# Kernel tuning notes

Measured on AMD Instinct MI355X. Metric: run time of the kernel, lower is better.

The kernel has to match this reference:

```python
import jax, jax.numpy as jnp
import numpy as np

NUM_HEADS = 32
HEAD_DIM = 128
HIDDEN = 4096
SEQ = 2048
BATCH = 1


def rotate_half(x):
    x1, x2 = jnp.split(x, 2, axis=-1)
    return jnp.concatenate((-x2, x1), axis=-1)


def rope_cos_sin(seq_len, dim, dtype=jnp.float32):
    inv_freq = 1.0 / (10000.0 ** (jnp.arange(0, dim, 2, dtype=jnp.float32) / dim))
    t = jnp.arange(seq_len, dtype=jnp.float32)
    freqs = jnp.einsum('i,j->ij', t, inv_freq)          # [S, dim/2]
    emb = jnp.concatenate((freqs, freqs), axis=-1)       # [S, dim]
    return jnp.cos(emb).astype(dtype), jnp.sin(emb).astype(dtype)


def setup_inputs() -> dict:
    key = jax.random.key(0)
    ks = jax.random.split(key, 6)
    s = 1.0 / np.sqrt(HIDDEN)
    return {
        'hidden_states': jax.random.normal(ks[0], (BATCH, SEQ, HIDDEN), jnp.float32),
        'attention_mask': jnp.ones((BATCH, SEQ), jnp.int32),
        'Wq': jax.random.normal(ks[1], (HIDDEN, HIDDEN), jnp.float32) * s,
        'Wk': jax.random.normal(ks[2], (HIDDEN, HIDDEN), jnp.float32) * s,
        'Wv': jax.random.normal(ks[3], (HIDDEN, HIDDEN), jnp.float32) * s,
        'Wo': jax.random.normal(ks[4], (HIDDEN, HIDDEN), jnp.float32) * s,
        'latent_queries': jax.random.normal(ks[5], (1, SEQ, HIDDEN), jnp.float32) * s,
    }


def reference(hidden_states, attention_mask, Wq, Wk, Wv, Wo, latent_queries):
    B, S, H = hidden_states.shape
    hd = HEAD_DIM
    scaling = hd ** -0.5

    def split_heads(x):  # [B,S,H] -> [B,nh,S,hd]
        return x.reshape(B, S, NUM_HEADS, hd).transpose(0, 2, 1, 3)

    k = split_heads(hidden_states @ Wk.T)
    v = split_heads(hidden_states @ Wv.T)

    cos, sin = rope_cos_sin(S, hd, hidden_states.dtype)  # [S,hd]
    cos = cos[None, None]
    sin = sin[None, None]
    k = k * cos + rotate_half(k) * sin  # rotated q is dead code in the original

    latents = jnp.broadcast_to(latent_queries[:, :S, :], (B, S, H))
    latent_q = split_heads(latents @ Wq.T)

    scores = jnp.einsum('bhqd,bhkd->bhqk', latent_q, k) * scaling
    mask = attention_mask[:, None, None, :] == 0
    scores = jnp.where(mask, -jnp.inf, scores)
    attn = jax.nn.softmax(scores.astype(jnp.float32), axis=-1).astype(hidden_states.dtype)
    # dropout is identity in eval mode
    out = jnp.einsum('bhqk,bhkd->bhqd', attn, v)
    out = out.transpose(0, 2, 1, 3).reshape(B, S, H)
    return out @ Wo.T
```

## Files before the change

### kernel.cpp

```cpp
#include <hip/hip_runtime.h>
#include <cstdint>
#include <type_traits>

typedef short bf16x8 __attribute__((ext_vector_type(8)));
typedef float f32x4 __attribute__((ext_vector_type(4)));

__device__ __forceinline__ ushort f2bf(float f) {
  union { float f; uint32_t u; } v; v.f = f;
  return (ushort)((v.u + 0x7fffu + ((v.u >> 16) & 1u)) >> 16);
}
__device__ __forceinline__ float bf2f(ushort u) {
  union { uint32_t u; float f; } v; v.u = ((uint32_t)u) << 16;
  return v.f;
}
__device__ __forceinline__ uint32_t pkbf(float x, float y) {
  uint32_t ux = (__float_as_uint(x) + 0x8000u) >> 16;
  uint32_t uy = (__float_as_uint(y) + 0x8000u) & 0xffff0000u;
  return ux | uy;
}

__device__ __forceinline__ void gld16(const void* g, void* l) {
  __builtin_amdgcn_global_load_lds(
      (__attribute__((address_space(1))) void*)(g),
      (__attribute__((address_space(3))) void*)(l), 16, 0, 0);
}

__device__ __forceinline__ uint4 ld8(const ushort* p) { return *(const uint4*)p; }
__device__ __forceinline__ uint4 ld8(const float* p) {
  float4 a = *(const float4*)p;
  float4 b = *(const float4*)(p + 4);
  uint4 r;
  r.x = pkbf(a.x, a.y); r.y = pkbf(a.z, a.w);
  r.z = pkbf(b.x, b.y); r.w = pkbf(b.z, b.w);
  return r;
}

__global__ __launch_bounds__(256) void cvt_bf16(
    const float* __restrict__ src, ushort* __restrict__ dst, int n8)
{
  int i = blockIdx.x * 256 + threadIdx.x;
  if (i >= n8) return;
  const float4* s = (const float4*)src;
  float4 a = s[2 * i], b = s[2 * i + 1];
  uint4 r;
  r.x = pkbf(a.x, a.y); r.y = pkbf(a.z, a.w);
  r.z = pkbf(b.x, b.y); r.w = pkbf(b.z, b.w);
  ((uint4*)dst)[i] = r;
}


#define BARw() __builtin_amdgcn_s_barrier()
#define LGKMW() do { asm volatile("s_waitcnt lgkmcnt(0)" ::: "memory"); \
                     __builtin_amdgcn_sched_barrier(0); } while (0)
#define VM6() asm volatile("s_waitcnt vmcnt(6)" ::: "memory")
#define VM0() asm volatile("s_waitcnt vmcnt(0)" ::: "memory")

__device__ __forceinline__ void stage_half8(
    const ushort* __restrict__ G, int row0, int col0,
    ushort* lds, int wave, int r4, int c8s)
{
#pragma unroll
  for (int q = 0; q < 2; ++q) {
    const int si = q * 8 + wave;
    const ushort* g = G + (size_t)(row0 + (si >> 1) * 16 + r4) * 4096
                        + (col0 + (si & 1) * 32 + c8s);
    gld16(g, lds + si * 512);
  }
}

__device__ __forceinline__ void read_a8(const ushort* base, int wm, int l16,
                                        int qsw, bf16x8 (&a)[4][2])
{
#pragma unroll
  for (int f = 0; f < 4; ++f)
#pragma unroll
    for (int ks = 0; ks < 2; ++ks)
      a[f][ks] = *(const bf16x8*)(base + ((wm * 4 + f) * 2 + ks) * 512
                                       + l16 * 32 + qsw);
}

__device__ __forceinline__ void read_b8(const ushort* base, int wn, int l16,
                                        int qsw, bf16x8 (&b)[2][2])
{
#pragma unroll
  for (int f = 0; f < 2; ++f)
#pragma unroll
    for (int ks = 0; ks < 2; ++ks)
      b[f][ks] = *(const bf16x8*)(base + ((wn * 2 + f) * 2 + ks) * 512
                                       + l16 * 32 + qsw);
}

template <int MH, int NH>
__device__ __forceinline__ void mfma_quad(const bf16x8 (&a)[4][2],
                                          const bf16x8 (&b)[2][2],
                                          f32x4 (&acc)[8][4])
{
  __builtin_amdgcn_s_setprio(1);
#pragma unroll
  for (int ks = 0; ks < 2; ++ks)
#pragma unroll
    for (int f = 0; f < 4; ++f)
#pragma unroll
      for (int g = 0; g < 2; ++g)
        acc[MH * 4 + f][NH * 2 + g] = __builtin_amdgcn_mfma_f32_16x16x32_bf16(
            a[f][ks], b[g][ks], acc[MH * 4 + f][NH * 2 + g], 0, 0, 0);
  __builtin_amdgcn_s_setprio(0);
}

template <int NT, int MODE>
__global__ __launch_bounds__(512, 2) void gemm8(
    const ushort* __restrict__ A0, const ushort* __restrict__ A1,
    const ushort* __restrict__ B0, const ushort* __restrict__ B1,
    ushort* __restrict__ O0, ushort* __restrict__ O1, ushort* __restrict__ O2,
    float* __restrict__ PF)
{
  __shared__ __align__(16) ushort smem[65536];
#define LDSA(P, H) (smem + (P) * 32768 + (H) * 8192)
#define LDSB(P, H) (smem + (P) * 32768 + 16384 + (H) * 8192)

  const int tid  = threadIdx.x;
  const int wave = tid >> 6;
  const int lane = tid & 63;
  const int quad = lane >> 4;
  const int l16  = lane & 15;
  const int wm   = wave >> 2;
  const int wn   = wave & 3;
  const int r4   = lane >> 2;
  const int c8s  = (((lane & 3) ^ ((lane >> 3) & 3))) * 8;
  const int qsw  = (quad ^ ((l16 >> 1) & 3)) * 8;

  const int bid = blockIdx.x;
  const ushort* Ag; const ushort* Bg;
  int m0, n0, kbase = 0, route = 0, kz = 0;
  if constexpr (MODE == 0) {
    const int swz = (bid & 7) * 48 + (bid >> 3);
    const int xt  = swz % 48;
    m0 = (swz / 48) * 256;
    if (xt < 32) { Ag = A0; Bg = B0; n0 = xt * 256; }
    else         { Ag = A1; Bg = B1; n0 = (xt - 32) * 256; }
    route = (xt >= 32) ? 2 : (n0 >= 4096 ? 1 : 0);
  } else {
    const int swz = (bid & 7) * 32 + (bid >> 3);
    kz = swz >> 7;
    const int r = swz & 127;
    m0 = (r >> 4) * 256;
    n0 = (r & 15) * 256;
    kbase = kz * 2048;
    Ag = A0; Bg = B0;
  }

  f32x4 acc[8][4];
#pragma unroll
  for (int i = 0; i < 8; ++i)
#pragma unroll
    for (int j = 0; j < 4; ++j) acc[i][j] = {0.f, 0.f, 0.f, 0.f};

  bf16x8 a[4][2], b0[2][2], b1[2][2];

  stage_half8(Ag, m0,       kbase,      LDSA(0, 0), wave, r4, c8s);
  stage_half8(Bg, n0,       kbase,      LDSB(0, 0), wave, r4, c8s);
  stage_half8(Bg, n0 + 128, kbase,      LDSB(0, 1), wave, r4, c8s);
  stage_half8(Ag, m0 + 128, kbase,      LDSA(0, 1), wave, r4, c8s);
  stage_half8(Ag, m0,       kbase + 64, LDSA(1, 0), wave, r4, c8s);
  stage_half8(Bg, n0,       kbase + 64, LDSB(1, 0), wave, r4, c8s);
  stage_half8(Bg, n0 + 128, kbase + 64, LDSB(1, 1), wave, r4, c8s);
  VM6();
  BARw();

#pragma unroll 1
  for (int t = 0; t < NT; t += 2) {
    read_a8(LDSA(0, 0), wm, l16, qsw, a);
    read_b8(LDSB(0, 0), wn, l16, qsw, b0);
    stage_half8(Ag, m0 + 128, kbase + (t + 1) * 64, LDSA(1, 1), wave, r4, c8s);
    BARw(); LGKMW();
    mfma_quad<0, 0>(a, b0, acc);
    BARw();

    read_b8(LDSB(0, 1), wn, l16, qsw, b1);
    if (t < NT - 2) stage_half8(Ag, m0, kbase + (t + 2) * 64, LDSA(0, 0), wave, r4, c8s);
    BARw(); LGKMW();
    mfma_quad<0, 1>(a, b1, acc);
    BARw();

    read_a8(LDSA(0, 1), wm, l16, qsw, a);
    if (t < NT - 2) stage_half8(Bg, n0, kbase + (t + 2) * 64, LDSB(0, 0), wave, r4, c8s);
    BARw(); LGKMW();
    mfma_quad<1, 0>(a, b0, acc);
    BARw();

    if (t < NT - 2) stage_half8(Bg, n0 + 128, kbase + (t + 2) * 64, LDSB(0, 1), wave, r4, c8s);
    BARw(); LGKMW();
    mfma_quad<1, 1>(a, b1, acc);
    if (t < NT - 2) VM6(); else VM0();
    BARw();

    read_a8(LDSA(1, 0), wm, l16, qsw, a);
    read_b8(LDSB(1, 0), wn, l16, qsw, b0);
    if (t < NT - 2) stage_half8(Ag, m0 + 128, kbase + (t + 2) * 64, LDSA(0, 1), wave, r4, c8s);
    BARw(); LGKMW();
    mfma_quad<0, 0>(a, b0, acc);
    BARw();

    read_b8(LDSB(1, 1), wn, l16, qsw, b1);
    if (t < NT - 3) stage_half8(Ag, m0, kbase + (t + 3) * 64, LDSA(1, 0), wave, r4, c8s);
    BARw(); LGKMW();
    mfma_quad<0, 1>(a, b1, acc);
    BARw();

    read_a8(LDSA(1, 1), wm, l16, qsw, a);
    if (t < NT - 3) stage_half8(Bg, n0, kbase + (t + 3) * 64, LDSB(1, 0), wave, r4, c8s);
    BARw(); LGKMW();
    mfma_quad<1, 0>(a, b0, acc);
    BARw();

    if (t < NT - 3) stage_half8(Bg, n0 + 128, kbase + (t + 3) * 64, LDSB(1, 1), wave, r4, c8s);
    BARw(); LGKMW();
    mfma_quad<1, 1>(a, b1, acc);
    if (t < NT - 4) { VM6(); } else if (t < NT - 2) { VM0(); }
    BARw();
  }

  if constexpr (MODE == 0) {
#pragma unroll
    for (int fm = 0; fm < 8; ++fm) {
      const int rowb = m0 + (fm >> 2) * 128 + wm * 64 + (fm & 3) * 16 + quad * 4;
#pragma unroll
      for (int fn = 0; fn < 4; ++fn) {
        const int col = n0 + (fn >> 1) * 128 + wn * 32 + (fn & 1) * 16 + l16;
#pragma unroll
        for (int r = 0; r < 4; ++r) {
          const ushort val = f2bf(acc[fm][fn][r]);
          const int row = rowb + r;
          if (route == 0)      O0[(size_t)row * 4096 + col] = val;
          else if (route == 1) O1[(size_t)(col - 4096) * 2048 + row] = val;
          else                 O2[(size_t)row * 4096 + col] = val;
        }
      }
    }
  } else {
    float* myP = PF + (size_t)kz * 2048 * 4096;
#pragma unroll
    for (int fm = 0; fm < 8; ++fm) {
      const int rowb = m0 + (fm >> 2) * 128 + wm * 64 + (fm & 3) * 16 + quad * 4;
#pragma unroll
      for (int fn = 0; fn < 4; ++fn) {
        const int col = n0 + (fn >> 1) * 128 + wn * 32 + (fn & 1) * 16 + l16;
#pragma unroll
        for (int r = 0; r < 4; ++r)
          myP[(size_t)(rowb + r) * 4096 + col] = acc[fm][fn][r];
      }
    }
  }
#undef LDSA
#undef LDSB
}

__global__ __launch_bounds__(256) void reduce2(
    const float* __restrict__ P, float* __restrict__ out, int n4)
{
  int i = blockIdx.x * 256 + threadIdx.x;
  if (i >= n4) return;
  const float4* p0 = (const float4*)P;
  const float4* p1 = (const float4*)(P + (size_t)2048 * 4096);
  float4 a = p0[i], b = p1[i];
  float4 r; r.x = a.x + b.x; r.y = a.y + b.y; r.z = a.z + b.z; r.w = a.w + b.w;
  ((float4*)out)[i] = r;
}

template <bool TRANSC, typename TA, typename TB, typename TC>
__global__ __launch_bounds__(256) void gemm_bt(
    const TA* __restrict__ A, const TB* __restrict__ B,
    TC* __restrict__ C, int M, int N, int K, int ldc)
{
  __shared__ __align__(16) ushort As[128 * 32];
  __shared__ __align__(16) ushort Bs[128 * 32];

  const int tid  = threadIdx.x;
  const int wave = tid >> 6;
  const int lane = tid & 63;
  const int quad = lane >> 4;
  const int l16  = lane & 15;
  const int m0 = blockIdx.y * 128;
  const int n0 = blockIdx.x * 128;
  const int wm = (wave & 1) * 64;
  const int wn = (wave >> 1) * 64;
  const int r0 = tid >> 2;
  const int c0 = (tid & 3) * 8;

  f32x4 acc[4][4];
#pragma unroll
  for (int i = 0; i < 4; i++)
#pragma unroll
    for (int j = 0; j < 4; j++) acc[i][j] = {0.f, 0.f, 0.f, 0.f};

  const TA* aptr = A + (size_t)(m0 + r0) * K + c0;
  const TB* bptr = B + (size_t)(n0 + r0) * K + c0;

  for (int k0 = 0; k0 < K; k0 += 32) {
    uint4 av0 = ld8(aptr + k0);
    uint4 av1 = ld8(aptr + (size_t)64 * K + k0);
    uint4 bv0 = ld8(bptr + k0);
    uint4 bv1 = ld8(bptr + (size_t)64 * K + k0);
    __syncthreads();
    *(uint4*)(As + r0 * 32 + c0)        = av0;
    *(uint4*)(As + (r0 + 64) * 32 + c0) = av1;
    *(uint4*)(Bs + r0 * 32 + c0)        = bv0;
    *(uint4*)(Bs + (r0 + 64) * 32 + c0) = bv1;
    __syncthreads();

    bf16x8 af[4], bfr[4];
#pragma unroll
    for (int i = 0; i < 4; i++) {
      af[i]  = *(const bf16x8*)(As + (wm + i * 16 + l16) * 32 + quad * 8);
      bfr[i] = *(const bf16x8*)(Bs + (wn + i * 16 + l16) * 32 + quad * 8);
    }
#pragma unroll
    for (int im = 0; im < 4; im++)
#pragma unroll
      for (int in = 0; in < 4; in++)
        acc[im][in] = __builtin_amdgcn_mfma_f32_16x16x32_bf16(
            af[im], bfr[in], acc[im][in], 0, 0, 0);
  }

#pragma unroll
  for (int im = 0; im < 4; im++)
#pragma unroll
    for (int in = 0; in < 4; in++)
#pragma unroll
      for (int r = 0; r < 4; r++) {
        int row = m0 + wm + im * 16 + quad * 4 + r;
        int col = n0 + wn + in * 16 + l16;
        float fv = acc[im][in][r];
        TC val;
        if constexpr (std::is_same<TC, ushort>::value) val = f2bf(fv);
        else                                           val = fv;
        if (TRANSC) C[(size_t)col * ldc + row] = val;
        else        C[(size_t)row * ldc + col] = val;
      }
}

__global__ __launch_bounds__(256) void rope_kernel(ushort* __restrict__ Kb)
{
  int idx = blockIdx.x * 256 + threadIdx.x;
  int j  = idx & 63;
  int hs = idx >> 6;
  int s  = hs >> 5;
  float freq = expf(-0.14391156f * (float)j);
  float ang  = (float)s * freq;
  float sn, c;
  sincosf(ang, &sn, &c);
  size_t base = (size_t)hs * 128 + j;
  float k1 = bf2f(Kb[base]);
  float k2 = bf2f(Kb[base + 64]);
  Kb[base]      = f2bf(k1 * c - k2 * sn);
  Kb[base + 64] = f2bf(k2 * c + k1 * sn);
}

__global__ __launch_bounds__(512, 2) void flash_attn(
    const ushort* __restrict__ Q, const ushort* __restrict__ Kb,
    const ushort* __restrict__ Vt, ushort* __restrict__ AO)
{
  __shared__ __align__(16) ushort Kt[128 * 128];
  __shared__ __align__(16) ushort Vs[128 * 128];
  __shared__ __align__(16) ushort Ps[8][16 * 128];

  const int tid  = threadIdx.x;
  const int wave = tid >> 6;
  const int lane = tid & 63;
  const int quad = lane >> 4;
  const int l16  = lane & 15;
  const int h  = blockIdx.y;
  const int q0 = blockIdx.x * 128 + wave * 16;
  const float scale = 0.08838834764831845f;

  bf16x8 aq[4];
#pragma unroll
  for (int kt = 0; kt < 4; kt++)
    aq[kt] = *(const bf16x8*)(Q + (size_t)(q0 + l16) * 4096 + h * 128 + kt * 32 + quad * 8);

  f32x4 Oacc[8];
#pragma unroll
  for (int dt = 0; dt < 8; dt++) Oacc[dt] = {0.f, 0.f, 0.f, 0.f};
  float m_i[4], l_i[4];
#pragma unroll
  for (int r = 0; r < 4; r++) { m_i[r] = -1e30f; l_i[r] = 0.f; }

  ushort* myP = &Ps[wave][0];

  uint4 kr[4], vr[4];
#pragma unroll
  for (int it = 0; it < 4; ++it) {
    int i = tid + it * 512;
    int row = i >> 4, g = i & 15;
    kr[it] = *(const uint4*)(Kb + (size_t)row * 4096 + h * 128 + g * 8);
    vr[it] = *(const uint4*)(Vt + (size_t)(h * 128 + row) * 2048 + g * 8);
  }

  for (int kv = 0; kv < 2048; kv += 128) {
    __syncthreads();
#pragma unroll
    for (int it = 0; it < 4; ++it) {
      int i = tid + it * 512;
      int row = i >> 4, g = i & 15;
      int sw = (g ^ (row & 15)) * 8;
      *(uint4*)(Kt + row * 128 + sw) = kr[it];
      *(uint4*)(Vs + row * 128 + sw) = vr[it];
    }
    __syncthreads();

    if (kv + 128 < 2048) {
#pragma unroll
      for (int it = 0; it < 4; ++it) {
        int i = tid + it * 512;
        int row = i >> 4, g = i & 15;
        kr[it] = *(const uint4*)(Kb + (size_t)(kv + 128 + row) * 4096 + h * 128 + g * 8);
        vr[it] = *(const uint4*)(Vt + (size_t)(h * 128 + row) * 2048 + kv + 128 + g * 8);
      }
    }

    f32x4 sA[8];
#pragma unroll
    for (int nt = 0; nt < 8; nt++) sA[nt] = {0.f, 0.f, 0.f, 0.f};
    __builtin_amdgcn_s_setprio(1);
#pragma unroll
    for (int nt = 0; nt < 8; nt++) {
      int row = nt * 16 + l16;
#pragma unroll
      for (int kt = 0; kt < 4; kt++) {
        int g = kt * 4 + quad;
        bf16x8 bk = *(const bf16x8*)(Kt + row * 128 + ((g ^ (row & 15)) * 8));
        sA[nt] = __builtin_amdgcn_mfma_f32_16x16x32_bf16(aq[kt], bk, sA[nt], 0, 0, 0);
      }
    }
    __builtin_amdgcn_s_setprio(0);

    float tmax[4];
#pragma unroll
    for (int r = 0; r < 4; r++) {
      float m = sA[0][r];
#pragma unroll
      for (int nt = 1; nt < 8; nt++) m = fmaxf(m, sA[nt][r]);
      tmax[r] = m;
    }
#pragma unroll
    for (int msk = 1; msk < 16; msk <<= 1)
#pragma unroll
      for (int r = 0; r < 4; r++)
        tmax[r] = fmaxf(tmax[r], __shfl_xor(tmax[r], msk));

    float nm[4];
    float growth = -1e30f;
#pragma unroll
    for (int r = 0; r < 4; r++) {
      nm[r] = tmax[r] * scale;
      growth = fmaxf(growth, nm[r] - m_i[r]);
    }
    if (__any(growth > 8.0f)) {
#pragma unroll
      for (int r = 0; r < 4; r++) {
        float mn = fmaxf(m_i[r], nm[r]);
        float al = __expf(m_i[r] - mn);
        m_i[r] = mn;
        l_i[r] *= al;
#pragma unroll
        for (int dt = 0; dt < 8; dt++) Oacc[dt][r] *= al;
      }
    }

    float rsum[4] = {0.f, 0.f, 0.f, 0.f};
#pragma unroll
    for (int nt = 0; nt < 8; nt++)
#pragma unroll
      for (int r = 0; r < 4; r++) {
        float p = __expf(sA[nt][r] * scale - m_i[r]);
        sA[nt][r] = p;
        rsum[r] += p;
      }
#pragma unroll
    for (int msk = 1; msk < 16; msk <<= 1)
#pragma unroll
      for (int r = 0; r < 4; r++) rsum[r] += __shfl_xor(rsum[r], msk);
#pragma unroll
    for (int r = 0; r < 4; r++) l_i[r] += rsum[r];

#pragma unroll
    for (int nt = 0; nt < 8; nt++)
#pragma unroll
      for (int r = 0; r < 4; r++) {
        int row = quad * 4 + r;
        int col = nt * 16 + l16;
        myP[row * 128 + (((col >> 3) ^ row) * 8) + (col & 7)] = f2bf(sA[nt][r]);
      }

    __builtin_amdgcn_s_setprio(1);
#pragma unroll
    for (int kt = 0; kt < 4; kt++) {
      int g = kt * 4 + quad;
      bf16x8 ap = *(const bf16x8*)(myP + l16 * 128 + ((g ^ l16) * 8));
#pragma unroll
      for (int dt = 0; dt < 8; dt++) {
        int vrow = dt * 16 + l16;
        bf16x8 bv = *(const bf16x8*)(Vs + vrow * 128 + ((g ^ (vrow & 15)) * 8));
        Oacc[dt] = __builtin_amdgcn_mfma_f32_16x16x32_bf16(ap, bv, Oacc[dt], 0, 0, 0);
      }
    }
    __builtin_amdgcn_s_setprio(0);
  }

#pragma unroll
  for (int dt = 0; dt < 8; dt++)
#pragma unroll
    for (int r = 0; r < 4; r++) {
      int row = q0 + quad * 4 + r;
      int col = h * 128 + dt * 16 + l16;
      AO[(size_t)row * 4096 + col] = f2bf(Oacc[dt][r] / l_i[r]);
    }
}

extern "C" void kernel_launch(void* const* d_in, const int* in_sizes, int n_in,
                              void* d_out, int out_size, void* d_ws, size_t ws_size,
                              hipStream_t stream)
{
  const float* hidden  = (const float*)d_in[0];
  const float* Wq      = (const float*)d_in[2];
  const float* Wk      = (const float*)d_in[3];
  const float* Wv      = (const float*)d_in[4];
  const float* Wo      = (const float*)d_in[5];
  const float* latents = (const float*)d_in[6];
  float* out = (float*)d_out;

  const size_t SB = (size_t)2048 * 4096 * 2;
  char* w = (char*)d_ws;
  const int n8_act = 2048 * 4096 / 8;
  const int n8_wt  = 4096 * 4096 / 8;

  if (ws_size >= 13 * SB) {
    ushort* hb  = (ushort*)(w);
    ushort* lb  = (ushort*)(w + 1 * SB);
    ushort* wqb = (ushort*)(w + 2 * SB);
    ushort* wkv = (ushort*)(w + 4 * SB);
    ushort* wob = (ushort*)(w + 8 * SB);
    ushort* Qb  = (ushort*)(w + 10 * SB);
    ushort* Kbf = (ushort*)(w + 11 * SB);
    ushort* Vtb = (ushort*)(w + 12 * SB);
    ushort* AOb = wqb;
    float*  Pp  = (float*)(w + 4 * SB);

    cvt_bf16<<<n8_act / 256, 256, 0, stream>>>(hidden,  hb,  n8_act);
    cvt_bf16<<<n8_act / 256, 256, 0, stream>>>(latents, lb,  n8_act);
    cvt_bf16<<<n8_wt / 256, 256, 0, stream>>>(Wq, wqb, n8_wt);
    cvt_bf16<<<n8_wt / 256, 256, 0, stream>>>(Wk, wkv, n8_wt);
    cvt_bf16<<<n8_wt / 256, 256, 0, stream>>>(Wv, wkv + (size_t)4096 * 4096, n8_wt);
    cvt_bf16<<<n8_wt / 256, 256, 0, stream>>>(Wo, wob, n8_wt);

    gemm8<64, 0><<<dim3(384), 512, 0, stream>>>(hb, lb, wkv, wqb, Kbf, Vtb, Qb, nullptr);
    rope_kernel<<<(2048 * 32 * 64) / 256, 256, 0, stream>>>(Kbf);
    flash_attn<<<dim3(16, 32), 512, 0, stream>>>(Qb, Kbf, Vtb, AOb);
    gemm8<32, 1><<<dim3(256), 512, 0, stream>>>(AOb, AOb, wob, wob,
                                                nullptr, nullptr, nullptr, Pp);
    reduce2<<<(2048 * 4096 / 4 + 255) / 256, 256, 0, stream>>>(Pp, out, 2048 * 4096 / 4);
  } else {
    ushort* Qb  = (ushort*)(w);
    ushort* Kbf = (ushort*)(w + 1 * SB);
    ushort* Vtb = (ushort*)(w + 2 * SB);
    ushort* AOb = (ushort*)(w + 3 * SB);

    gemm_bt<false><<<dim3(32, 16), 256, 0, stream>>>(latents, Wq, Qb, 2048, 4096, 4096, 4096);
    gemm_bt<false><<<dim3(32, 16), 256, 0, stream>>>(hidden, Wk, Kbf, 2048, 4096, 4096, 4096);
    gemm_bt<true><<<dim3(32, 16), 256, 0, stream>>>(hidden, Wv, Vtb, 2048, 4096, 4096, 2048);
    rope_kernel<<<(2048 * 32 * 64) / 256, 256, 0, stream>>>(Kbf);
    flash_attn<<<dim3(16, 32), 512, 0, stream>>>(Qb, Kbf, Vtb, AOb);
    gemm_bt<false><<<dim3(32, 16), 256, 0, stream>>>(AOb, Wo, out, 2048, 4096, 4096, 4096);
  }
}
```

Baseline: 809.8 us.

## Shrink GEMM block tile from 256x256 to 128x256 and simplify pipeline

Halves the M dimension of the gemm8 block tile, so the QKV and output-projection GEMMs launch twice as many blocks and each block keeps half the accumulators. The 8-phase double-buffer loop becomes a 2-phase loop per K step with smaller LDS staging (96KB instead of 128KB). The aim is better occupancy and load balance across CUs, possibly higher waves per CU from fewer registers, in exchange for lower arithmetic intensity per tile and more global/LDS traffic for B.

```diff
diff --git a/kernel.cpp b/kernel.cpp
--- a/kernel.cpp
+++ b/kernel.cpp
@@ -52,7 +52,7 @@
 #define BARw() __builtin_amdgcn_s_barrier()
 #define LGKMW() do { asm volatile("s_waitcnt lgkmcnt(0)" ::: "memory"); \
                      __builtin_amdgcn_sched_barrier(0); } while (0)
-#define VM6() asm volatile("s_waitcnt vmcnt(6)" ::: "memory")
+#define VM4() asm volatile("s_waitcnt vmcnt(4)" ::: "memory")
 #define VM0() asm volatile("s_waitcnt vmcnt(0)" ::: "memory")
 
 __device__ __forceinline__ void stage_half8(
@@ -90,10 +90,10 @@
                                        + l16 * 32 + qsw);
 }
 
-template <int MH, int NH>
-__device__ __forceinline__ void mfma_quad(const bf16x8 (&a)[4][2],
+template <int NH>
+__device__ __forceinline__ void mfma_half(const bf16x8 (&a)[4][2],
                                           const bf16x8 (&b)[2][2],
-                                          f32x4 (&acc)[8][4])
+                                          f32x4 (&acc)[4][4])
 {
   __builtin_amdgcn_s_setprio(1);
 #pragma unroll
@@ -102,8 +102,8 @@
     for (int f = 0; f < 4; ++f)
 #pragma unroll
       for (int g = 0; g < 2; ++g)
-        acc[MH * 4 + f][NH * 2 + g] = __builtin_amdgcn_mfma_f32_16x16x32_bf16(
-            a[f][ks], b[g][ks], acc[MH * 4 + f][NH * 2 + g], 0, 0, 0);
+        acc[f][NH * 2 + g] = __builtin_amdgcn_mfma_f32_16x16x32_bf16(
+            a[f][ks], b[g][ks], acc[f][NH * 2 + g], 0, 0, 0);
   __builtin_amdgcn_s_setprio(0);
 }
 
@@ -114,9 +114,9 @@
     ushort* __restrict__ O0, ushort* __restrict__ O1, ushort* __restrict__ O2,
     float* __restrict__ PF)
 {
-  __shared__ __align__(16) ushort smem[65536];
-#define LDSA(P, H) (smem + (P) * 32768 + (H) * 8192)
-#define LDSB(P, H) (smem + (P) * 32768 + 16384 + (H) * 8192)
+  __shared__ __align__(16) ushort smem[49152];
+#define LDSA(P)    (smem + (P) * 24576)
+#define LDSB(P, H) (smem + (P) * 24576 + 8192 + (H) * 8192)
 
   const int tid  = threadIdx.x;
   const int wave = tid >> 6;
@@ -133,97 +133,64 @@
   const ushort* Ag; const ushort* Bg;
   int m0, n0, kbase = 0, route = 0, kz = 0;
   if constexpr (MODE == 0) {
-    const int swz = (bid & 7) * 48 + (bid >> 3);
+    const int swz = (bid & 7) * 96 + (bid >> 3);
     const int xt  = swz % 48;
-    m0 = (swz / 48) * 256;
+    m0 = (swz / 48) * 128;
     if (xt < 32) { Ag = A0; Bg = B0; n0 = xt * 256; }
     else         { Ag = A1; Bg = B1; n0 = (xt - 32) * 256; }
     route = (xt >= 32) ? 2 : (n0 >= 4096 ? 1 : 0);
   } else {
-    const int swz = (bid & 7) * 32 + (bid >> 3);
-    kz = swz >> 7;
-    const int r = swz & 127;
-    m0 = (r >> 4) * 256;
+    const int swz = (bid & 7) * 64 + (bid >> 3);
+    kz = swz >> 8;
+    const int r = swz & 255;
+    m0 = (r >> 4) * 128;
     n0 = (r & 15) * 256;
     kbase = kz * 2048;
     Ag = A0; Bg = B0;
   }
 
-  f32x4 acc[8][4];
-#pragma unroll
-  for (int i = 0; i < 8; ++i)
+  f32x4 acc[4][4];
+#pragma unroll
+  for (int i = 0; i < 4; ++i)
 #pragma unroll
     for (int j = 0; j < 4; ++j) acc[i][j] = {0.f, 0.f, 0.f, 0.f};
 
   bf16x8 a[4][2], b0[2][2], b1[2][2];
 
-  stage_half8(Ag, m0,       kbase,      LDSA(0, 0), wave, r4, c8s);
+  stage_half8(Ag, m0,       kbase,      LDSA(0),    wave, r4, c8s);
   stage_half8(Bg, n0,       kbase,      LDSB(0, 0), wave, r4, c8s);
   stage_half8(Bg, n0 + 128, kbase,      LDSB(0, 1), wave, r4, c8s);
-  stage_half8(Ag, m0 + 128, kbase,      LDSA(0, 1), wave, r4, c8s);
-  stage_half8(Ag, m0,       kbase + 64, LDSA(1, 0), wave, r4, c8s);
+  stage_half8(Ag, m0,       kbase + 64, LDSA(1),    wave, r4, c8s);
   stage_half8(Bg, n0,       kbase + 64, LDSB(1, 0), wave, r4, c8s);
-  stage_half8(Bg, n0 + 128, kbase + 64, LDSB(1, 1), wave, r4, c8s);
-  VM6();
+  VM4();
   BARw();
 
 #pragma unroll 1
-  for (int t = 0; t < NT; t += 2) {
-    read_a8(LDSA(0, 0), wm, l16, qsw, a);
-    read_b8(LDSB(0, 0), wn, l16, qsw, b0);
-    stage_half8(Ag, m0 + 128, kbase + (t + 1) * 64, LDSA(1, 1), wave, r4, c8s);
+  for (int t = 0; t < NT; ++t) {
+    const int p = t & 1;
+    read_a8(LDSA(p), wm, l16, qsw, a);
+    read_b8(LDSB(p, 0), wn, l16, qsw, b0);
+    if (t + 1 < NT)
+      stage_half8(Bg, n0 + 128, kbase + (t + 1) * 64, LDSB(p ^ 1, 1), wave, r4, c8s);
     BARw(); LGKMW();
-    mfma_quad<0, 0>(a, b0, acc);
+    mfma_half<0>(a, b0, acc);
     BARw();
 
-    read_b8(LDSB(0, 1), wn, l16, qsw, b1);
-    if (t < NT - 2) stage_half8(Ag, m0, kbase + (t + 2) * 64, LDSA(0, 0), wave, r4, c8s);
+    read_b8(LDSB(p, 1), wn, l16, qsw, b1);
+    if (t + 2 < NT) {
+      stage_half8(Ag, m0, kbase + (t + 2) * 64, LDSA(p),    wave, r4, c8s);
+      stage_half8(Bg, n0, kbase + (t + 2) * 64, LDSB(p, 0), wave, r4, c8s);
+    }
     BARw(); LGKMW();
-    mfma_quad<0, 1>(a, b1, acc);
+    mfma_half<1>(a, b1, acc);
+    if (t + 2 < NT) { VM4(); } else if (t + 1 < NT) { VM0(); }
     BARw();
-
-    read_a8(LDSA(0, 1), wm, l16, qsw, a);
-    if (t < NT - 2) stage_half8(Bg, n0, kbase + (t + 2) * 64, LDSB(0, 0), wave, r4, c8s);
-    BARw(); LGKMW();
-    mfma_quad<1, 0>(a, b0, acc);
-    BARw();
-
-    if (t < NT - 2) stage_half8(Bg, n0 + 128, kbase + (t + 2) * 64, LDSB(0, 1), wave, r4, c8s);
-    BARw(); LGKMW();
-    mfma_quad<1, 1>(a, b1, acc);
-    if (t < NT - 2) VM6(); else VM0();
-    BARw();
-
-    read_a8(LDSA(1, 0), wm, l16, qsw, a);
-    read_b8(LDSB(1, 0), wn, l16, qsw, b0);
-    if (t < NT - 2) stage_half8(Ag, m0 + 128, kbase + (t + 2) * 64, LDSA(0, 1), wave, r4, c8s);
-    BARw(); LGKMW();
-    mfma_quad<0, 0>(a, b0, acc);
-    BARw();
-
-    read_b8(LDSB(1, 1), wn, l16, qsw, b1);
-    if (t < NT - 3) stage_half8(Ag, m0, kbase + (t + 3) * 64, LDSA(1, 0), wave, r4, c8s);
-    BARw(); LGKMW();
-    mfma_quad<0, 1>(a, b1, acc);
-    BARw();
-
-    read_a8(LDSA(1, 1), wm, l16, qsw, a);
-    if (t < NT - 3) stage_half8(Bg, n0, kbase + (t + 3) * 64, LDSB(1, 0), wave, r4, c8s);
-    BARw(); LGKMW();
-    mfma_quad<1, 0>(a, b0, acc);
-    BARw();
-
-    if (t < NT - 3) stage_half8(Bg, n0 + 128, kbase + (t + 3) * 64, LDSB(1, 1), wave, r4, c8s);
-    BARw(); LGKMW();
-    mfma_quad<1, 1>(a, b1, acc);
-    if (t < NT - 4) { VM6(); } else if (t < NT - 2) { VM0(); }
-    BARw();
   }
 
   if constexpr (MODE == 0) {
 #pragma unroll
-    for (int fm = 0; fm < 8; ++fm) {
-      const int rowb = m0 + (fm >> 2) * 128 + wm * 64 + (fm & 3) * 16 + quad * 4;
+    for (int fm = 0; fm < 4; ++fm) {
+      const int rowb = m0 + wm * 64 + fm * 16 + quad * 4;
 #pragma unroll
       for (int fn = 0; fn < 4; ++fn) {
         const int col = n0 + (fn >> 1) * 128 + wn * 32 + (fn & 1) * 16 + l16;
@@ -240,8 +207,8 @@
   } else {
     float* myP = PF + (size_t)kz * 2048 * 4096;
 #pragma unroll
-    for (int fm = 0; fm < 8; ++fm) {
-      const int rowb = m0 + (fm >> 2) * 128 + wm * 64 + (fm & 3) * 16 + quad * 4;
+    for (int fm = 0; fm < 4; ++fm) {
+      const int rowb = m0 + wm * 64 + fm * 16 + quad * 4;
 #pragma unroll
       for (int fn = 0; fn < 4; ++fn) {
         const int col = n0 + (fn >> 1) * 128 + wn * 32 + (fn & 1) * 16 + l16;
@@ -553,10 +520,10 @@
     cvt_bf16<<<n8_wt / 256, 256, 0, stream>>>(Wv, wkv + (size_t)4096 * 4096, n8_wt);
     cvt_bf16<<<n8_wt / 256, 256, 0, stream>>>(Wo, wob, n8_wt);
 
-    gemm8<64, 0><<<dim3(384), 512, 0, stream>>>(hb, lb, wkv, wqb, Kbf, Vtb, Qb, nullptr);
+    gemm8<64, 0><<<dim3(768), 512, 0, stream>>>(hb, lb, wkv, wqb, Kbf, Vtb, Qb, nullptr);
     rope_kernel<<<(2048 * 32 * 64) / 256, 256, 0, stream>>>(Kbf);
     flash_attn<<<dim3(16, 32), 512, 0, stream>>>(Qb, Kbf, Vtb, AOb);
-    gemm8<32, 1><<<dim3(256), 512, 0, stream>>>(AOb, AOb, wob, wob,
+    gemm8<32, 1><<<dim3(512), 512, 0, stream>>>(AOb, AOb, wob, wob,
                                                 nullptr, nullptr, nullptr, Pp);
     reduce2<<<(2048 * 4096 / 4 + 255) / 256, 256, 0, stream>>>(Pp, out, 2048 * 4096 / 4);
   } else {
```

Result: slower. 841.3 us (+3.9%).
